# Optimization experiments

Hardware: AMD Instinct MI355X
Metric: run time of the kernel (lower is better)

Reference implementation:

```python
import jax, jax.numpy as jnp
import numpy as np
from jax import lax

L, D, V, T = 12, 1024, 50277, 1024
F4 = 4 * D


def setup_inputs() -> dict:
    key = jax.random.key(0)
    ks = jax.random.split(key, 20)
    s = 0.02  # weight scale keeps k (exp argument) well-conditioned
    n = lambda k, shape, scale=s: jax.random.normal(k, shape, dtype=jnp.float32) * scale
    u = lambda k, shape: jax.random.uniform(k, shape, dtype=jnp.float32)
    return {
        "tokens": jax.random.randint(ks[0], (T,), 0, V, dtype=jnp.int32),
        "emb": n(ks[1], (V, D), 1.0),
        "ln0_w": jnp.ones((D,), jnp.float32), "ln0_b": jnp.zeros((D,), jnp.float32),
        "ln1_w": jnp.ones((L, D), jnp.float32), "ln1_b": jnp.zeros((L, D), jnp.float32),
        "ln2_w": jnp.ones((L, D), jnp.float32), "ln2_b": jnp.zeros((L, D), jnp.float32),
        "tmk": u(ks[2], (L, D)), "tmv": u(ks[3], (L, D)), "tmr": u(ks[4], (L, D)),
        "tmk_ffn": u(ks[5], (L, D)), "tmr_ffn": u(ks[6], (L, D)),
        "time_first": n(ks[7], (L, D), 0.5),
        "time_decay": -jnp.exp(n(ks[8], (L, D), 0.5)),  # __init__: -exp(raw)
        "att_kw": n(ks[9], (L, D, D)), "att_vw": n(ks[10], (L, D, D)),
        "att_rw": n(ks[11], (L, D, D)), "att_ow": n(ks[12], (L, D, D)),
        "ffn_kw": n(ks[13], (L, D, F4)), "ffn_vw": n(ks[14], (L, F4, D)),
        "ffn_rw": n(ks[15], (L, D, D)),
        "lnout_w": jnp.ones((D,), jnp.float32), "lnout_b": jnp.zeros((D,), jnp.float32),
        "head": n(ks[16], (V, D)),
    }


def _ln(x, w, b):
    mu = jnp.mean(x, -1, keepdims=True)
    var = jnp.var(x, -1, keepdims=True)
    return (x - mu) / jnp.sqrt(var + 1e-5) * w + b


def _shift(x):  # token shift: prepend zero state row (state init is zeros)
    return jnp.concatenate([jnp.zeros_like(x[:1]), x[:-1]], axis=0)


def _wkv(k, v, tf, td):  # k,v: [T,D]; aa/bb/pp scan with running-max exp trick
    init = (jnp.zeros_like(k[0]), jnp.zeros_like(k[0]), jnp.full_like(k[0], -1e30))
    def step(c, kv):
        aa, bb, pp = c
        kt, vt = kv
        ww = tf + kt
        p = jnp.maximum(pp, ww)
        e1 = jnp.exp(pp - p); e2 = jnp.exp(ww - p)
        out = (e1 * aa + e2 * vt) / (e1 * bb + e2)
        ww2 = pp + td
        p2 = jnp.maximum(ww2, kt)
        e1 = jnp.exp(ww2 - p2); e2 = jnp.exp(kt - p2)
        return (e1 * aa + e2 * vt, e1 * bb + e2, p2), out
    _, out = lax.scan(step, init, (k, v))
    return out


def reference(tokens, emb, ln0_w, ln0_b, ln1_w, ln1_b, ln2_w, ln2_b, tmk, tmv, tmr,
              tmk_ffn, tmr_ffn, time_first, time_decay, att_kw, att_vw, att_rw, att_ow,
              ffn_kw, ffn_vw, ffn_rw, lnout_w, lnout_b, head):
    x = _ln(emb[tokens], ln0_w, ln0_b)  # [T,D]; ln0 applied to emb rows as in __init__
    for i in range(L):
        # time-mix (attention) block
        xn = _ln(x, ln1_w[i], ln1_b[i])
        xx = _shift(xn)
        xk = xn * tmk[i] + xx * (1 - tmk[i])
        xv = xn * tmv[i] + xx * (1 - tmv[i])
        xr = xn * tmr[i] + xx * (1 - tmr[i])
        r = jax.nn.sigmoid(xr @ att_rw[i])
        k = xk @ att_kw[i]
        v = xv @ att_vw[i]
        wkv = _wkv(k, v, time_first[i], time_decay[i])
        x = x + (r * wkv) @ att_ow[i]
        # channel-mix (ffn) block
        xn = _ln(x, ln2_w[i], ln2_b[i])
        xx = _shift(xn)
        xk = xn * tmk_ffn[i] + xx * (1 - tmk_ffn[i])
        xr = xn * tmr_ffn[i] + xx * (1 - tmr_ffn[i])
        rf = jax.nn.sigmoid(xr @ ffn_rw[i])
        kf = jnp.square(jax.nn.relu(xk @ ffn_kw[i]))
        x = x + rf * (kf @ ffn_vw[i])
    xo = _ln(x[-1], lnout_w, lnout_b)
    return head @ xo  # logits [V]
```

## Files before the change

kernel.cpp:

```cpp
#include <hip/hip_runtime.h>

#define Tn 1024
#define Dn 1024
#define Ln 12
#define F4n 4096
#define Vn 50277
#define TDn (Tn*Dn)
#define MEG 1048576
#define SEG 16
#define NSEG 64

typedef __attribute__((ext_vector_type(4))) float f4;
typedef __attribute__((ext_vector_type(16))) float f32x16;
typedef __attribute__((ext_vector_type(8))) short short8;
typedef unsigned short u16;
typedef unsigned int u32;
typedef __attribute__((ext_vector_type(4))) u16 us4;

#define ASG __attribute__((address_space(1)))
#define ASL __attribute__((address_space(3)))

__device__ __forceinline__ u16 f2b(float x){
  u32 u = __float_as_uint(x);
  return (u16)((u + 0x7fffu + ((u >> 16) & 1u)) >> 16);
}

__device__ __forceinline__ f4 blockReduce4(f4 v){
  __shared__ f4 s[4];
  int lane = threadIdx.x & 63, w = threadIdx.x >> 6;
#pragma unroll
  for(int o = 32; o; o >>= 1){
    v.x += __shfl_xor(v.x, o);
    v.y += __shfl_xor(v.y, o);
    v.z += __shfl_xor(v.z, o);
    v.w += __shfl_xor(v.w, o);
  }
  if(lane == 0) s[w] = v;
  __syncthreads();
  return s[0] + s[1] + s[2] + s[3];
}

struct ConvArgs {
  const float* s0; const float* s1; const float* s2; const float* s3;
  const float* skw;
  const float* svw;
  const float* srw;
  u16* dst;
};
__global__ __launch_bounds__(256) void conv_k(ConvArgs a){
  __shared__ u16 t[64][65];
  int b = blockIdx.x, tid = threadIdx.x;
  const float* src; u16* dst; int K, N, tk, tn;
  if(b < 1024){
    int m = b >> 8, bt = b & 255;
    src = (m==0)?a.s0:((m==1)?a.s1:((m==2)?a.s2:a.s3));
    dst = a.dst + (size_t)m*MEG; K=1024; N=1024; tk=bt>>4; tn=bt&15;
  } else if(b < 2048){
    int bt = b-1024; src=a.skw; dst=a.dst+(size_t)4*MEG; K=1024; N=4096; tk=bt>>6; tn=bt&63;
  } else if(b < 3072){
    int bt = b-2048; src=a.svw; dst=a.dst+(size_t)8*MEG; K=4096; N=1024; tk=bt>>4; tn=bt&15;
  } else {
    int bt = b-3072; src=a.srw; dst=a.dst+(size_t)12*MEG; K=1024; N=1024; tk=bt>>4; tn=bt&15;
  }
  int r0 = tid>>6, c = tid&63;
#pragma unroll
  for(int it=0; it<16; it++){
    int r = it*4 + r0;
    t[r][c] = f2b(src[(size_t)(tk*64+r)*N + tn*64 + c]);
  }
  __syncthreads();
  int n0 = tid>>4, k4 = (tid&15)*4;
#pragma unroll
  for(int it=0; it<4; it++){
    int n = it*16 + n0;
    us4 o; o[0]=t[k4][n]; o[1]=t[k4+1][n]; o[2]=t[k4+2][n]; o[3]=t[k4+3][n];
    *(us4*)&dst[(size_t)(tn*64+n)*K + tk*64 + k4] = o;
  }
}

__global__ __launch_bounds__(256) void embed_ln0_k(
    const int* __restrict__ tok, const float* __restrict__ emb,
    const float* __restrict__ w, const float* __restrict__ b,
    float* __restrict__ x){
  int t = blockIdx.x, tid = threadIdx.x;
  const f4* src = (const f4*)(emb + (size_t)tok[t] * Dn);
  f4 v = src[tid];
  f4 st;
  st.x = v.x+v.y+v.z+v.w;
  st.y = v.x*v.x+v.y*v.y+v.z*v.z+v.w*v.w;
  st.z = 0.f; st.w = 0.f;
  f4 red = blockReduce4(st);
  float mu = red.x * (1.0f/Dn);
  float rs = rsqrtf(red.y * (1.0f/Dn) - mu*mu + 1e-5f);
  f4 wv = ((const f4*)w)[tid], bv = ((const f4*)b)[tid];
  f4 o;
  o.x = (v.x-mu)*rs*wv.x + bv.x;
  o.y = (v.y-mu)*rs*wv.y + bv.y;
  o.z = (v.z-mu)*rs*wv.z + bv.z;
  o.w = (v.w-mu)*rs*wv.w + bv.w;
  ((f4*)(x + (size_t)t*Dn))[tid] = o;
}

__global__ __launch_bounds__(256) void ln_mix_att_k(
    const float* __restrict__ x,
    const float* __restrict__ lw, const float* __restrict__ lb,
    const float* __restrict__ tk, const float* __restrict__ tv, const float* __restrict__ tr,
    u16* __restrict__ xkvr){
  int t = blockIdx.x, tid = threadIdx.x;
  f4 cur = ((const f4*)(x + (size_t)t*Dn))[tid];
  f4 prv; prv.x=0.f; prv.y=0.f; prv.z=0.f; prv.w=0.f;
  if(t > 0) prv = ((const f4*)(x + (size_t)(t-1)*Dn))[tid];
  f4 st;
  st.x = cur.x+cur.y+cur.z+cur.w;
  st.y = cur.x*cur.x+cur.y*cur.y+cur.z*cur.z+cur.w*cur.w;
  st.z = prv.x+prv.y+prv.z+prv.w;
  st.w = prv.x*prv.x+prv.y*prv.y+prv.z*prv.z+prv.w*prv.w;
  f4 red = blockReduce4(st);
  float muc = red.x*(1.f/Dn), rsc = rsqrtf(red.y*(1.f/Dn)-muc*muc+1e-5f);
  float mup = red.z*(1.f/Dn), rsp = rsqrtf(red.w*(1.f/Dn)-mup*mup+1e-5f);
  f4 wv=((const f4*)lw)[tid], bv=((const f4*)lb)[tid];
  f4 kv=((const f4*)tk)[tid], vv=((const f4*)tv)[tid], rv=((const f4*)tr)[tid];
  us4 ok, ov, orr;
  float xn, xp;
#define MIX3(j, cj, pj, wj, bj, kj, vj, rj) \
  xn = (cj - muc)*rsc*wj + bj; \
  xp = (t>0) ? ((pj - mup)*rsp*wj + bj) : 0.f; \
  ok[j]  = f2b(xn*kj + xp*(1.f-kj)); \
  ov[j]  = f2b(xn*vj + xp*(1.f-vj)); \
  orr[j] = f2b(xn*rj + xp*(1.f-rj));
  MIX3(0, cur.x, prv.x, wv.x, bv.x, kv.x, vv.x, rv.x)
  MIX3(1, cur.y, prv.y, wv.y, bv.y, kv.y, vv.y, rv.y)
  MIX3(2, cur.z, prv.z, wv.z, bv.z, kv.z, vv.z, rv.z)
  MIX3(3, cur.w, prv.w, wv.w, bv.w, kv.w, vv.w, rv.w)
#undef MIX3
  size_t o0 = (size_t)t*Dn + tid*4;
  *(us4*)(xkvr + o0)         = ok;
  *(us4*)(xkvr + TDn + o0)   = ov;
  *(us4*)(xkvr + 2*TDn + o0) = orr;
}

__global__ __launch_bounds__(256) void ln_mix_ffn_k(
    const float* __restrict__ x,
    const float* __restrict__ lw, const float* __restrict__ lb,
    const float* __restrict__ tk, const float* __restrict__ tr,
    u16* __restrict__ xkr){
  int t = blockIdx.x, tid = threadIdx.x;
  f4 cur = ((const f4*)(x + (size_t)t*Dn))[tid];
  f4 prv; prv.x=0.f; prv.y=0.f; prv.z=0.f; prv.w=0.f;
  if(t > 0) prv = ((const f4*)(x + (size_t)(t-1)*Dn))[tid];
  f4 st;
  st.x = cur.x+cur.y+cur.z+cur.w;
  st.y = cur.x*cur.x+cur.y*cur.y+cur.z*cur.z+cur.w*cur.w;
  st.z = prv.x+prv.y+prv.z+prv.w;
  st.w = prv.x*prv.x+prv.y*prv.y+prv.z*prv.z+prv.w*prv.w;
  f4 red = blockReduce4(st);
  float muc = red.x*(1.f/Dn), rsc = rsqrtf(red.y*(1.f/Dn)-muc*muc+1e-5f);
  float mup = red.z*(1.f/Dn), rsp = rsqrtf(red.w*(1.f/Dn)-mup*mup+1e-5f);
  f4 wv=((const f4*)lw)[tid], bv=((const f4*)lb)[tid];
  f4 kv=((const f4*)tk)[tid], rv=((const f4*)tr)[tid];
  us4 ok, orr;
  float xn, xp;
#define MIX2(j, cj, pj, wj, bj, kj, rj) \
  xn = (cj - muc)*rsc*wj + bj; \
  xp = (t>0) ? ((pj - mup)*rsp*wj + bj) : 0.f; \
  ok[j]  = f2b(xn*kj + xp*(1.f-kj)); \
  orr[j] = f2b(xn*rj + xp*(1.f-rj));
  MIX2(0, cur.x, prv.x, wv.x, bv.x, kv.x, rv.x)
  MIX2(1, cur.y, prv.y, wv.y, bv.y, kv.y, rv.y)
  MIX2(2, cur.z, prv.z, wv.z, bv.z, kv.z, rv.z)
  MIX2(3, cur.w, prv.w, wv.w, bv.w, kv.w, rv.w)
#undef MIX2
  size_t o0 = (size_t)t*Dn + tid*4;
  *(us4*)(xkr + o0)       = ok;
  *(us4*)(xkr + TDn + o0) = orr;
}

__global__ __launch_bounds__(256) void wkv_seg_k(
    const float* __restrict__ kb, const float* __restrict__ vb,
    const float* __restrict__ tdp,
    float* __restrict__ sega, float* __restrict__ segb, float* __restrict__ segp){
  int ch = blockIdx.x*256 + threadIdx.x;
  int g = blockIdx.y;
  int t0 = g*SEG;
  float td = tdp[ch];
  float kk[SEG], vv[SEG];
#pragma unroll
  for(int j=0;j<SEG;j++){
    kk[j] = kb[(size_t)(t0+j)*Dn + ch];
    vv[j] = vb[(size_t)(t0+j)*Dn + ch];
  }
  float aa=0.f, bb=0.f, pp=-1e30f;
#pragma unroll
  for(int j=0;j<SEG;j++){
    float ww2 = pp + td;
    float p2 = fmaxf(ww2, kk[j]);
    float e1 = __expf(ww2-p2), e2 = __expf(kk[j]-p2);
    aa = e1*aa + e2*vv[j]; bb = e1*bb + e2; pp = p2;
  }
  size_t o = (size_t)g*Dn + ch;
  sega[o] = aa; segb[o] = bb; segp[o] = pp;
}

__global__ __launch_bounds__(256) void wkv_scan_k(
    const float* __restrict__ sega, const float* __restrict__ segb, const float* __restrict__ segp,
    const float* __restrict__ tdp,
    float* __restrict__ prea, float* __restrict__ preb, float* __restrict__ prep){
  int ch = blockIdx.x*256 + threadIdx.x;
  float Std = tdp[ch] * (float)SEG;
  float a=0.f, b=0.f, p=-1e30f;
  for(int g=0; g<NSEG; g++){
    size_t o = (size_t)g*Dn + ch;
    prea[o]=a; preb[o]=b; prep[o]=p;
    float ag=sega[o], bg=segb[o], qg=segp[o];
    float psh = p + Std;
    float pn = fmaxf(psh, qg);
    float eo = __expf(psh-pn), en = __expf(qg-pn);
    a = eo*a + en*ag; b = eo*b + en*bg; p = pn;
  }
}

__global__ __launch_bounds__(256) void wkv_out_k(
    const float* __restrict__ kb, const float* __restrict__ vb, const float* __restrict__ rb,
    const float* __restrict__ tfp, const float* __restrict__ tdp,
    const float* __restrict__ prea, const float* __restrict__ preb, const float* __restrict__ prep,
    u16* __restrict__ att_in){
  int ch = blockIdx.x*256 + threadIdx.x;
  int g = blockIdx.y;
  int t0 = g*SEG;
  float tf = tfp[ch], td = tdp[ch];
  size_t so = (size_t)g*Dn + ch;
  float aa = prea[so], bb = preb[so], pp = prep[so];
  float kk[SEG], vv[SEG], rr[SEG];
#pragma unroll
  for(int j=0;j<SEG;j++){
    kk[j]=kb[(size_t)(t0+j)*Dn+ch];
    vv[j]=vb[(size_t)(t0+j)*Dn+ch];
    rr[j]=rb[(size_t)(t0+j)*Dn+ch];
  }
#pragma unroll
  for(int j=0;j<SEG;j++){
    float kt=kk[j], vt=vv[j];
    float ww = tf + kt;
    float p = fmaxf(pp, ww);
    float e1 = __expf(pp-p), e2 = __expf(ww-p);
    float out = __fdividef(e1*aa+e2*vt, e1*bb+e2);
    float sig = __fdividef(1.f, 1.f+__expf(-rr[j]));
    att_in[(size_t)(t0+j)*Dn+ch] = f2b(sig*out);
    float ww2 = pp+td;
    float p2 = fmaxf(ww2,kt);
    e1 = __expf(ww2-p2); e2 = __expf(kt-p2);
    aa = e1*aa+e2*vt; bb = e1*bb+e2; pp = p2;
  }
}

template<int EPI>
__global__ __launch_bounds__(128) void gemm_k(
    const u16* __restrict__ A, size_t ldA, size_t strideA,
    const u16* __restrict__ Bt, size_t ldB, size_t strideB,
    int K, int N,
    float* __restrict__ Cf, size_t strideC, u16* __restrict__ Cb,
    const float* __restrict__ aux){
  __shared__ __align__(16) u16 lds[2][2][64*128];
  const int tid = threadIdx.x;
  const int l = tid & 63, w = tid >> 6;
  const int z = blockIdx.z;
  const u16* Az = A  + (size_t)z*strideA;
  const u16* Bz = Bt + (size_t)z*strideB;
  const int row0 = blockIdx.y*64, col0 = blockIdx.x*64;

  const u16* pA[8]; const u16* pB[8]; int ldsoff[8];
#pragma unroll
  for(int q=0;q<8;q++){
    int r = (q*2+w)*4 + (l>>4);
    int kk = (((l&15)*16) ^ ((r&15)<<4)) >> 1;
    pA[q] = Az + (size_t)(row0+r)*ldA + kk;
    pB[q] = Bz + (size_t)(col0+r)*ldB + kk;
    ldsoff[q] = (q*2+w)*512;
  }
  int foff[2][4];
#pragma unroll
  for(int i=0;i<2;i++){
    int row = i*32 + (l&31);
#pragma unroll
    for(int s=0;s<4;s++){
      int c = w*128 + s*32 + ((l>>5)*16);
      foff[i][s] = row*128 + ((c ^ ((row&15)<<4)) >> 1);
    }
  }

  f32x16 acc[2][2];
#pragma unroll
  for(int i=0;i<2;i++)
#pragma unroll
    for(int j=0;j<2;j++)
#pragma unroll
      for(int e=0;e<16;e++) acc[i][j][e] = 0.f;

#define STAGE(BUF) do{ \
  _Pragma("unroll") \
  for(int q=0;q<8;q++){ \
    __builtin_amdgcn_global_load_lds((ASG const void*)(const void*)pA[q], (ASL void*)(void*)&lds[BUF][0][ldsoff[q]], 16, 0, 0); \
    __builtin_amdgcn_global_load_lds((ASG const void*)(const void*)pB[q], (ASL void*)(void*)&lds[BUF][1][ldsoff[q]], 16, 0, 0); \
    pA[q] += 128; pB[q] += 128; \
  } }while(0)

  const int nss = K >> 7;
  STAGE(0);
  __syncthreads();
  int buf = 0;
  for(int ss=0; ss<nss; ss++){
    if(ss+1 < nss){
      if(buf) STAGE(0); else STAGE(1);
    }
    const u16* La = &lds[buf][0][0];
    const u16* Lb = &lds[buf][1][0];
#pragma unroll
    for(int s=0;s<4;s++){
      short8 a0 = *(const short8*)(La + foff[0][s]);
      short8 a1 = *(const short8*)(La + foff[1][s]);
      short8 b0 = *(const short8*)(Lb + foff[0][s]);
      short8 b1 = *(const short8*)(Lb + foff[1][s]);
      acc[0][0] = __builtin_amdgcn_mfma_f32_32x32x16_bf16(a0, b0, acc[0][0], 0, 0, 0);
      acc[0][1] = __builtin_amdgcn_mfma_f32_32x32x16_bf16(a0, b1, acc[0][1], 0, 0, 0);
      acc[1][0] = __builtin_amdgcn_mfma_f32_32x32x16_bf16(a1, b0, acc[1][0], 0, 0, 0);
      acc[1][1] = __builtin_amdgcn_mfma_f32_32x32x16_bf16(a1, b1, acc[1][1], 0, 0, 0);
    }
    __syncthreads();
    buf ^= 1;
  }
#undef STAGE

  float* red = (float*)&lds[0][0][0];
  if(w == 1){
#pragma unroll
    for(int i=0;i<2;i++)
#pragma unroll
      for(int j=0;j<2;j++)
#pragma unroll
        for(int reg=0;reg<16;reg++){
          int rr_ = (reg&3) + 8*(reg>>2) + 4*(l>>5);
          red[(size_t)(i*32 + rr_)*64 + j*32 + (l&31)] = acc[i][j][reg];
        }
  }
  __syncthreads();
  if(w == 0){
#pragma unroll
    for(int i=0;i<2;i++)
#pragma unroll
      for(int j=0;j<2;j++)
#pragma unroll
        for(int reg=0;reg<16;reg++){
          int rr_ = (reg&3) + 8*(reg>>2) + 4*(l>>5);
          float v = acc[i][j][reg] + red[(size_t)(i*32 + rr_)*64 + j*32 + (l&31)];
          int grow = row0 + i*32 + rr_;
          int gcol = col0 + j*32 + (l&31);
          size_t idx = (size_t)grow*N + gcol;
          if constexpr(EPI==0){ Cf[(size_t)z*strideC + idx] = v; }
          else if constexpr(EPI==1){ float t_ = v>0.f ? v : 0.f; Cb[idx] = f2b(t_*t_); }
          else if constexpr(EPI==2){ Cf[idx] += v; }
          else { float s_ = __fdividef(1.f, 1.f+__expf(-aux[idx])); Cf[idx] += s_*v; }
        }
  }
}

__global__ __launch_bounds__(256) void lnout_k(
    const float* __restrict__ x, const float* __restrict__ w, const float* __restrict__ b,
    float* __restrict__ xo){
  int tid = threadIdx.x;
  f4 v = ((const f4*)(x + (size_t)(Tn-1)*Dn))[tid];
  f4 st;
  st.x = v.x+v.y+v.z+v.w;
  st.y = v.x*v.x+v.y*v.y+v.z*v.z+v.w*v.w;
  st.z = 0.f; st.w = 0.f;
  f4 red = blockReduce4(st);
  float mu = red.x*(1.f/Dn);
  float rs = rsqrtf(red.y*(1.f/Dn) - mu*mu + 1e-5f);
  f4 wv = ((const f4*)w)[tid], bv = ((const f4*)b)[tid];
  f4 o;
  o.x = (v.x-mu)*rs*wv.x + bv.x;
  o.y = (v.y-mu)*rs*wv.y + bv.y;
  o.z = (v.z-mu)*rs*wv.z + bv.z;
  o.w = (v.w-mu)*rs*wv.w + bv.w;
  ((f4*)xo)[tid] = o;
}

__global__ __launch_bounds__(256) void head_k(
    const float* __restrict__ head, const float* __restrict__ xo, float* __restrict__ out){
  __shared__ f4 sxo[256];
  int tid = threadIdx.x;
  sxo[tid] = ((const f4*)xo)[tid];
  __syncthreads();
  int w = tid >> 6, lane = tid & 63;
  int row = blockIdx.x*4 + w;
  if(row < Vn){
    const f4* hr = (const f4*)(head + (size_t)row*Dn);
    float s = 0.f;
#pragma unroll
    for(int i=0;i<4;i++){
      f4 h = hr[i*64 + lane];
      f4 xv = sxo[i*64 + lane];
      s += h.x*xv.x + h.y*xv.y + h.z*xv.z + h.w*xv.w;
    }
#pragma unroll
    for(int o=32;o;o>>=1) s += __shfl_xor(s, o);
    if(lane == 0) out[row] = s;
  }
}

static inline void launch_gemm(int epi, dim3 grid,
    const u16* A, size_t ldA, size_t sA,
    const u16* Bt, size_t ldB, size_t sB,
    int K, int N,
    float* Cf, size_t sC, u16* Cb, const float* aux, hipStream_t s){
  switch(epi){
    case 0: gemm_k<0><<<grid, 128, 0, s>>>(A, ldA, sA, Bt, ldB, sB, K, N, Cf, sC, Cb, aux); break;
    case 1: gemm_k<1><<<grid, 128, 0, s>>>(A, ldA, sA, Bt, ldB, sB, K, N, Cf, sC, Cb, aux); break;
    case 2: gemm_k<2><<<grid, 128, 0, s>>>(A, ldA, sA, Bt, ldB, sB, K, N, Cf, sC, Cb, aux); break;
    default: gemm_k<3><<<grid, 128, 0, s>>>(A, ldA, sA, Bt, ldB, sB, K, N, Cf, sC, Cb, aux); break;
  }
}

extern "C" void kernel_launch(void* const* d_in, const int* in_sizes, int n_in,
                              void* d_out, int out_size, void* d_ws, size_t ws_size,
                              hipStream_t stream) {
  (void)in_sizes; (void)n_in; (void)out_size; (void)ws_size;
  const int*   tokens   = (const int*)  d_in[0];
  const float* emb      = (const float*)d_in[1];
  const float* ln0_w    = (const float*)d_in[2];
  const float* ln0_b    = (const float*)d_in[3];
  const float* ln1_w    = (const float*)d_in[4];
  const float* ln1_b    = (const float*)d_in[5];
  const float* ln2_w    = (const float*)d_in[6];
  const float* ln2_b    = (const float*)d_in[7];
  const float* tmk      = (const float*)d_in[8];
  const float* tmv      = (const float*)d_in[9];
  const float* tmr      = (const float*)d_in[10];
  const float* tmk_ffn  = (const float*)d_in[11];
  const float* tmr_ffn  = (const float*)d_in[12];
  const float* tfirst   = (const float*)d_in[13];
  const float* tdecay   = (const float*)d_in[14];
  const float* att_kw   = (const float*)d_in[15];
  const float* att_vw   = (const float*)d_in[16];
  const float* att_rw   = (const float*)d_in[17];
  const float* att_ow   = (const float*)d_in[18];
  const float* ffn_kw   = (const float*)d_in[19];
  const float* ffn_vw   = (const float*)d_in[20];
  const float* ffn_rw   = (const float*)d_in[21];
  const float* lnoutw   = (const float*)d_in[22];
  const float* lnoutb   = (const float*)d_in[23];
  const float* headw    = (const float*)d_in[24];
  float* logits = (float*)d_out;

  char* wsb = (char*)d_ws;
  size_t off = 0;
  auto carve = [&](size_t bytes)->void*{
    void* p = wsb + off;
    off += (bytes + 255) & ~(size_t)255;
    return p;
  };
  float* x      = (float*)carve((size_t)TDn*4);
  u16*   xkvr   = (u16*)  carve((size_t)3*TDn*2);
  float* kvr    = (float*)carve((size_t)3*TDn*4);
  u16*   att_in = (u16*)  carve((size_t)TDn*2);
  u16*   xkr    = (u16*)  carve((size_t)2*TDn*2);
  u16*   kf     = (u16*)  carve((size_t)Tn*F4n*2);
  float* rf     = (float*)carve((size_t)TDn*4);
  float* xo     = (float*)carve((size_t)Dn*4);
  u16*   wbt    = (u16*)  carve((size_t)13*MEG*2);
  float* sega   = (float*)carve((size_t)NSEG*Dn*4);
  float* segb   = (float*)carve((size_t)NSEG*Dn*4);
  float* segp   = (float*)carve((size_t)NSEG*Dn*4);
  float* prea   = (float*)carve((size_t)NSEG*Dn*4);
  float* preb   = (float*)carve((size_t)NSEG*Dn*4);
  float* prep   = (float*)carve((size_t)NSEG*Dn*4);

  embed_ln0_k<<<Tn, 256, 0, stream>>>(tokens, emb, ln0_w, ln0_b, x);

  for(int i=0;i<Ln;i++){
    size_t dd = (size_t)i*Dn*Dn;
    ConvArgs ca;
    ca.s0 = att_kw+dd; ca.s1 = att_vw+dd; ca.s2 = att_rw+dd; ca.s3 = att_ow+dd;
    ca.skw = ffn_kw+(size_t)i*Dn*F4n; ca.svw = ffn_vw+(size_t)i*F4n*Dn; ca.srw = ffn_rw+dd;
    ca.dst = wbt;
    conv_k<<<3328, 256, 0, stream>>>(ca);

    ln_mix_att_k<<<Tn, 256, 0, stream>>>(x, ln1_w+i*Dn, ln1_b+i*Dn,
                                         tmk+i*Dn, tmv+i*Dn, tmr+i*Dn, xkvr);
    launch_gemm(0, dim3(16,16,3), xkvr, Dn, (size_t)TDn,
                wbt, Dn, (size_t)MEG, Dn, Dn,
                kvr, (size_t)TDn, nullptr, nullptr, stream);
    wkv_seg_k<<<dim3(4,NSEG), 256, 0, stream>>>(kvr, kvr+TDn, tdecay+i*Dn, sega, segb, segp);
    wkv_scan_k<<<4, 256, 0, stream>>>(sega, segb, segp, tdecay+i*Dn, prea, preb, prep);
    wkv_out_k<<<dim3(4,NSEG), 256, 0, stream>>>(kvr, kvr+TDn, kvr+2*TDn,
                                                tfirst+i*Dn, tdecay+i*Dn,
                                                prea, preb, prep, att_in);
    launch_gemm(2, dim3(16,16,1), att_in, Dn, 0,
                wbt+(size_t)3*MEG, Dn, 0, Dn, Dn,
                x, 0, nullptr, nullptr, stream);
    ln_mix_ffn_k<<<Tn, 256, 0, stream>>>(x, ln2_w+i*Dn, ln2_b+i*Dn,
                                         tmk_ffn+i*Dn, tmr_ffn+i*Dn, xkr);
    launch_gemm(1, dim3(64,16,1), xkr, Dn, 0,
                wbt+(size_t)4*MEG, Dn, 0, Dn, F4n,
                nullptr, 0, kf, nullptr, stream);
    launch_gemm(0, dim3(16,16,1), xkr+TDn, Dn, 0,
                wbt+(size_t)12*MEG, Dn, 0, Dn, Dn,
                rf, 0, nullptr, nullptr, stream);
    launch_gemm(3, dim3(16,16,1), kf, F4n, 0,
                wbt+(size_t)8*MEG, F4n, 0, F4n, Dn,
                x, 0, nullptr, rf, stream);
  }

  lnout_k<<<1, 256, 0, stream>>>(x, lnoutw, lnoutb, xo);
  head_k<<<(Vn+3)/4, 256, 0, stream>>>(headw, xo, logits);
}
```

Measured before the change: 1.943 ms.

## Halve GEMM K-step to 64 and remap blocks for XCD-aware L2 locality

Shrinks the per-stage K tile in the bf16 MFMA GEMM from 128 to 64, halving LDS use per block, which may allow more resident blocks per CU. It also remaps the linear block index so that consecutive groups of column tiles land on the same one of 8 chiplets (XCDs). The goal is better L2 reuse of shared A/B tiles. The cost is twice as many K iterations and barriers per tile, and the remap assumes gridDim.x is divisible by 8.

```diff
diff --git a/kernel.cpp b/kernel.cpp
--- a/kernel.cpp
+++ b/kernel.cpp
@@ -260,31 +260,41 @@
     int K, int N,
     float* __restrict__ Cf, size_t strideC, u16* __restrict__ Cb,
     const float* __restrict__ aux){
-  __shared__ __align__(16) u16 lds[2][2][64*128];
+  __shared__ __align__(16) u16 lds[2][2][64*64];
   const int tid = threadIdx.x;
   const int l = tid & 63, w = tid >> 6;
-  const int z = blockIdx.z;
-  const u16* Az = A  + (size_t)z*strideA;
-  const u16* Bz = Bt + (size_t)z*strideB;
-  const int row0 = blockIdx.y*64, col0 = blockIdx.x*64;
-
-  const u16* pA[8]; const u16* pB[8]; int ldsoff[8];
-#pragma unroll
-  for(int q=0;q<8;q++){
-    int r = (q*2+w)*4 + (l>>4);
-    int kk = (((l&15)*16) ^ ((r&15)<<4)) >> 1;
+
+  const int GX = gridDim.x, GY = gridDim.y;
+  int lin = blockIdx.x + GX*(blockIdx.y + GY*blockIdx.z);
+  int c  = lin & 7, s = lin >> 3;
+  int XT = GX >> 3;
+  int tpz = XT * GY;
+  int tz  = s / tpz, rem = s - tz*tpz;
+  int tx  = c*XT + rem / GY;
+  int ty  = rem - (rem / GY)*GY;
+
+  const u16* Az = A  + (size_t)tz*strideA;
+  const u16* Bz = Bt + (size_t)tz*strideB;
+  const int row0 = ty*64, col0 = tx*64;
+
+  const u16* pA[4]; const u16* pB[4]; int ldsoff[4];
+#pragma unroll
+  for(int q=0;q<4;q++){
+    int ch = q*2 + w;
+    int r  = ch*8 + (l>>3);
+    int kk = ((((l&7)<<4) ^ ((l>>3)<<4)) >> 1);
     pA[q] = Az + (size_t)(row0+r)*ldA + kk;
     pB[q] = Bz + (size_t)(col0+r)*ldB + kk;
-    ldsoff[q] = (q*2+w)*512;
-  }
-  int foff[2][4];
+    ldsoff[q] = ch*512;
+  }
+  int foff[2][2];
 #pragma unroll
   for(int i=0;i<2;i++){
     int row = i*32 + (l&31);
 #pragma unroll
-    for(int s=0;s<4;s++){
-      int c = w*128 + s*32 + ((l>>5)*16);
-      foff[i][s] = row*128 + ((c ^ ((row&15)<<4)) >> 1);
+    for(int s2=0;s2<2;s2++){
+      int cb = w*64 + s2*32 + ((l>>5)*16);
+      foff[i][s2] = row*64 + ((cb ^ ((row&7)<<4)) >> 1);
     }
   }
 
@@ -298,13 +308,13 @@
 
 #define STAGE(BUF) do{ \
   _Pragma("unroll") \
-  for(int q=0;q<8;q++){ \
+  for(int q=0;q<4;q++){ \
     __builtin_amdgcn_global_load_lds((ASG const void*)(const void*)pA[q], (ASL void*)(void*)&lds[BUF][0][ldsoff[q]], 16, 0, 0); \
     __builtin_amdgcn_global_load_lds((ASG const void*)(const void*)pB[q], (ASL void*)(void*)&lds[BUF][1][ldsoff[q]], 16, 0, 0); \
-    pA[q] += 128; pB[q] += 128; \
+    pA[q] += 64; pB[q] += 64; \
   } }while(0)
 
-  const int nss = K >> 7;
+  const int nss = K >> 6;
   STAGE(0);
   __syncthreads();
   int buf = 0;
@@ -315,11 +325,11 @@
     const u16* La = &lds[buf][0][0];
     const u16* Lb = &lds[buf][1][0];
 #pragma unroll
-    for(int s=0;s<4;s++){
-      short8 a0 = *(const short8*)(La + foff[0][s]);
-      short8 a1 = *(const short8*)(La + foff[1][s]);
-      short8 b0 = *(const short8*)(Lb + foff[0][s]);
-      short8 b1 = *(const short8*)(Lb + foff[1][s]);
+    for(int s2=0;s2<2;s2++){
+      short8 a0 = *(const short8*)(La + foff[0][s2]);
+      short8 a1 = *(const short8*)(La + foff[1][s2]);
+      short8 b0 = *(const short8*)(Lb + foff[0][s2]);
+      short8 b1 = *(const short8*)(Lb + foff[1][s2]);
       acc[0][0] = __builtin_amdgcn_mfma_f32_32x32x16_bf16(a0, b0, acc[0][0], 0, 0, 0);
       acc[0][1] = __builtin_amdgcn_mfma_f32_32x32x16_bf16(a0, b1, acc[0][1], 0, 0, 0);
       acc[1][0] = __builtin_amdgcn_mfma_f32_32x32x16_bf16(a1, b0, acc[1][0], 0, 0, 0);
@@ -355,7 +365,7 @@
           int grow = row0 + i*32 + rr_;
           int gcol = col0 + j*32 + (l&31);
           size_t idx = (size_t)grow*N + gcol;
-          if constexpr(EPI==0){ Cf[(size_t)z*strideC + idx] = v; }
+          if constexpr(EPI==0){ Cf[(size_t)tz*strideC + idx] = v; }
           else if constexpr(EPI==1){ float t_ = v>0.f ? v : 0.f; Cb[idx] = f2b(t_*t_); }
           else if constexpr(EPI==2){ Cf[idx] += v; }
           else { float s_ = __fdividef(1.f, 1.f+__expf(-aux[idx])); Cf[idx] += s_*v; }
```

After: 2.018 ms. 3.8% more time.

## Batch weight conversion, fuse WKV scan into output, merge FFN key/receptance GEMMs

Applied to the files above, without the earlier changes.

Converts all twelve layers' weights to transposed bf16 in one launch before the layer loop, instead of one conversion launch per layer. The separate serial WKV segment-scan kernel is removed: each output block now recomputes its own prefix over earlier segments. The FFN key and receptance GEMMs run as a single launch with branch-selected epilogues. This cuts launch count and serialization, and raises occupancy for the small receptance GEMM. In exchange it needs a much larger bf16 weight workspace and adds redundant prefix-scan work that grows with segment index.

```diff
diff --git a/kernel.cpp b/kernel.cpp
--- a/kernel.cpp
+++ b/kernel.cpp
@@ -9,6 +9,7 @@
 #define MEG 1048576
 #define SEG 16
 #define NSEG 64
+#define WL (13*MEG)
 
 typedef __attribute__((ext_vector_type(4))) float f4;
 typedef __attribute__((ext_vector_type(16))) float f32x16;
@@ -41,26 +42,27 @@
 }
 
 struct ConvArgs {
-  const float* s0; const float* s1; const float* s2; const float* s3;
-  const float* skw;
-  const float* svw;
-  const float* srw;
+  const float* akw; const float* avw; const float* arw; const float* aow;
+  const float* fkw; const float* fvw; const float* frw;
   u16* dst;
 };
 __global__ __launch_bounds__(256) void conv_k(ConvArgs a){
   __shared__ u16 t[64][65];
-  int b = blockIdx.x, tid = threadIdx.x;
+  int b = blockIdx.x, L = blockIdx.y, tid = threadIdx.x;
   const float* src; u16* dst; int K, N, tk, tn;
+  size_t lyr_dd = (size_t)L*MEG;
+  size_t lyr_f4 = (size_t)L*4*MEG;
+  u16* dl = a.dst + (size_t)L*WL;
   if(b < 1024){
     int m = b >> 8, bt = b & 255;
-    src = (m==0)?a.s0:((m==1)?a.s1:((m==2)?a.s2:a.s3));
-    dst = a.dst + (size_t)m*MEG; K=1024; N=1024; tk=bt>>4; tn=bt&15;
+    src = ((m==0)?a.akw:((m==1)?a.avw:((m==2)?a.arw:a.aow))) + lyr_dd;
+    dst = dl + (size_t)m*MEG; K=1024; N=1024; tk=bt>>4; tn=bt&15;
   } else if(b < 2048){
-    int bt = b-1024; src=a.skw; dst=a.dst+(size_t)4*MEG; K=1024; N=4096; tk=bt>>6; tn=bt&63;
+    int bt = b-1024; src=a.fkw+lyr_f4; dst=dl+(size_t)4*MEG; K=1024; N=4096; tk=bt>>6; tn=bt&63;
   } else if(b < 3072){
-    int bt = b-2048; src=a.svw; dst=a.dst+(size_t)8*MEG; K=4096; N=1024; tk=bt>>4; tn=bt&15;
+    int bt = b-2048; src=a.fvw+lyr_f4; dst=dl+(size_t)8*MEG; K=4096; N=1024; tk=bt>>4; tn=bt&15;
   } else {
-    int bt = b-3072; src=a.srw; dst=a.dst+(size_t)12*MEG; K=1024; N=1024; tk=bt>>4; tn=bt&15;
+    int bt = b-3072; src=a.frw+lyr_dd; dst=dl+(size_t)12*MEG; K=1024; N=1024; tk=bt>>4; tn=bt&15;
   }
   int r0 = tid>>6, c = tid&63;
 #pragma unroll
@@ -201,35 +203,25 @@
   sega[o] = aa; segb[o] = bb; segp[o] = pp;
 }
 
-__global__ __launch_bounds__(256) void wkv_scan_k(
-    const float* __restrict__ sega, const float* __restrict__ segb, const float* __restrict__ segp,
-    const float* __restrict__ tdp,
-    float* __restrict__ prea, float* __restrict__ preb, float* __restrict__ prep){
-  int ch = blockIdx.x*256 + threadIdx.x;
-  float Std = tdp[ch] * (float)SEG;
-  float a=0.f, b=0.f, p=-1e30f;
-  for(int g=0; g<NSEG; g++){
-    size_t o = (size_t)g*Dn + ch;
-    prea[o]=a; preb[o]=b; prep[o]=p;
-    float ag=sega[o], bg=segb[o], qg=segp[o];
-    float psh = p + Std;
-    float pn = fmaxf(psh, qg);
-    float eo = __expf(psh-pn), en = __expf(qg-pn);
-    a = eo*a + en*ag; b = eo*b + en*bg; p = pn;
-  }
-}
-
-__global__ __launch_bounds__(256) void wkv_out_k(
+__global__ __launch_bounds__(256) void wkv_outscan_k(
     const float* __restrict__ kb, const float* __restrict__ vb, const float* __restrict__ rb,
     const float* __restrict__ tfp, const float* __restrict__ tdp,
-    const float* __restrict__ prea, const float* __restrict__ preb, const float* __restrict__ prep,
+    const float* __restrict__ sega, const float* __restrict__ segb, const float* __restrict__ segp,
     u16* __restrict__ att_in){
   int ch = blockIdx.x*256 + threadIdx.x;
   int g = blockIdx.y;
   int t0 = g*SEG;
   float tf = tfp[ch], td = tdp[ch];
-  size_t so = (size_t)g*Dn + ch;
-  float aa = prea[so], bb = preb[so], pp = prep[so];
+  float Std = td * (float)SEG;
+  float aa=0.f, bb=0.f, pp=-1e30f;
+  for(int j=0;j<g;j++){
+    size_t o = (size_t)j*Dn + ch;
+    float ag=sega[o], bg=segb[o], qg=segp[o];
+    float psh = pp + Std;
+    float pn = fmaxf(psh, qg);
+    float eo = __expf(psh-pn), en = __expf(qg-pn);
+    aa = eo*aa + en*ag; bb = eo*bb + en*bg; pp = pn;
+  }
   float kk[SEG], vv[SEG], rr[SEG];
 #pragma unroll
   for(int j=0;j<SEG;j++){
@@ -258,7 +250,7 @@
     const u16* __restrict__ A, size_t ldA, size_t strideA,
     const u16* __restrict__ Bt, size_t ldB, size_t strideB,
     int K, int N,
-    float* __restrict__ Cf, size_t strideC, u16* __restrict__ Cb,
+    float* __restrict__ Cf, size_t strideC,
     const float* __restrict__ aux){
   __shared__ __align__(16) u16 lds[2][2][64*128];
   const int tid = threadIdx.x;
@@ -356,9 +348,114 @@
           int gcol = col0 + j*32 + (l&31);
           size_t idx = (size_t)grow*N + gcol;
           if constexpr(EPI==0){ Cf[(size_t)z*strideC + idx] = v; }
-          else if constexpr(EPI==1){ float t_ = v>0.f ? v : 0.f; Cb[idx] = f2b(t_*t_); }
           else if constexpr(EPI==2){ Cf[idx] += v; }
           else { float s_ = __fdividef(1.f, 1.f+__expf(-aux[idx])); Cf[idx] += s_*v; }
+        }
+  }
+}
+
+__global__ __launch_bounds__(128) void gemm_fkr_k(
+    const u16* __restrict__ xkr, const u16* __restrict__ wl,
+    u16* __restrict__ kf, float* __restrict__ rf){
+  __shared__ __align__(16) u16 lds[2][2][64*128];
+  const int tid = threadIdx.x;
+  const int l = tid & 63, w = tid >> 6;
+  const bool isfk = blockIdx.x < 64;
+  const u16* Az = isfk ? xkr : xkr + TDn;
+  const u16* Bz = isfk ? wl + (size_t)4*MEG : wl + (size_t)12*MEG;
+  const int N = isfk ? F4n : Dn;
+  const int col0 = (isfk ? blockIdx.x : blockIdx.x-64)*64;
+  const int row0 = blockIdx.y*64;
+
+  const u16* pA[8]; const u16* pB[8]; int ldsoff[8];
+#pragma unroll
+  for(int q=0;q<8;q++){
+    int r = (q*2+w)*4 + (l>>4);
+    int kk = (((l&15)*16) ^ ((r&15)<<4)) >> 1;
+    pA[q] = Az + (size_t)(row0+r)*Dn + kk;
+    pB[q] = Bz + (size_t)(col0+r)*Dn + kk;
+    ldsoff[q] = (q*2+w)*512;
+  }
+  int foff[2][4];
+#pragma unroll
+  for(int i=0;i<2;i++){
+    int row = i*32 + (l&31);
+#pragma unroll
+    for(int s=0;s<4;s++){
+      int c = w*128 + s*32 + ((l>>5)*16);
+      foff[i][s] = row*128 + ((c ^ ((row&15)<<4)) >> 1);
+    }
+  }
+
+  f32x16 acc[2][2];
+#pragma unroll
+  for(int i=0;i<2;i++)
+#pragma unroll
+    for(int j=0;j<2;j++)
+#pragma unroll
+      for(int e=0;e<16;e++) acc[i][j][e] = 0.f;
+
+#define STAGE(BUF) do{ \
+  _Pragma("unroll") \
+  for(int q=0;q<8;q++){ \
+    __builtin_amdgcn_global_load_lds((ASG const void*)(const void*)pA[q], (ASL void*)(void*)&lds[BUF][0][ldsoff[q]], 16, 0, 0); \
+    __builtin_amdgcn_global_load_lds((ASG const void*)(const void*)pB[q], (ASL void*)(void*)&lds[BUF][1][ldsoff[q]], 16, 0, 0); \
+    pA[q] += 128; pB[q] += 128; \
+  } }while(0)
+
+  STAGE(0);
+  __syncthreads();
+  int buf = 0;
+#pragma unroll 1
+  for(int ss=0; ss<8; ss++){
+    if(ss+1 < 8){
+      if(buf) STAGE(0); else STAGE(1);
+    }
+    const u16* La = &lds[buf][0][0];
+    const u16* Lb = &lds[buf][1][0];
+#pragma unroll
+    for(int s=0;s<4;s++){
+      short8 a0 = *(const short8*)(La + foff[0][s]);
+      short8 a1 = *(const short8*)(La + foff[1][s]);
+      short8 b0 = *(const short8*)(Lb + foff[0][s]);
+      short8 b1 = *(const short8*)(Lb + foff[1][s]);
+      acc[0][0] = __builtin_amdgcn_mfma_f32_32x32x16_bf16(a0, b0, acc[0][0], 0, 0, 0);
+      acc[0][1] = __builtin_amdgcn_mfma_f32_32x32x16_bf16(a0, b1, acc[0][1], 0, 0, 0);
+      acc[1][0] = __builtin_amdgcn_mfma_f32_32x32x16_bf16(a1, b0, acc[1][0], 0, 0, 0);
+      acc[1][1] = __builtin_amdgcn_mfma_f32_32x32x16_bf16(a1, b1, acc[1][1], 0, 0, 0);
+    }
+    __syncthreads();
+    buf ^= 1;
+  }
+#undef STAGE
+
+  float* red = (float*)&lds[0][0][0];
+  if(w == 1){
+#pragma unroll
+    for(int i=0;i<2;i++)
+#pragma unroll
+      for(int j=0;j<2;j++)
+#pragma unroll
+        for(int reg=0;reg<16;reg++){
+          int rr_ = (reg&3) + 8*(reg>>2) + 4*(l>>5);
+          red[(size_t)(i*32 + rr_)*64 + j*32 + (l&31)] = acc[i][j][reg];
+        }
+  }
+  __syncthreads();
+  if(w == 0){
+#pragma unroll
+    for(int i=0;i<2;i++)
+#pragma unroll
+      for(int j=0;j<2;j++)
+#pragma unroll
+        for(int reg=0;reg<16;reg++){
+          int rr_ = (reg&3) + 8*(reg>>2) + 4*(l>>5);
+          float v = acc[i][j][reg] + red[(size_t)(i*32 + rr_)*64 + j*32 + (l&31)];
+          int grow = row0 + i*32 + rr_;
+          int gcol = col0 + j*32 + (l&31);
+          size_t idx = (size_t)grow*N + gcol;
+          if(isfk){ float t_ = v>0.f ? v : 0.f; kf[idx] = f2b(t_*t_); }
+          else rf[idx] = v;
         }
   }
 }
@@ -411,12 +508,11 @@
     const u16* A, size_t ldA, size_t sA,
     const u16* Bt, size_t ldB, size_t sB,
     int K, int N,
-    float* Cf, size_t sC, u16* Cb, const float* aux, hipStream_t s){
+    float* Cf, size_t sC, const float* aux, hipStream_t s){
   switch(epi){
-    case 0: gemm_k<0><<<grid, 128, 0, s>>>(A, ldA, sA, Bt, ldB, sB, K, N, Cf, sC, Cb, aux); break;
-    case 1: gemm_k<1><<<grid, 128, 0, s>>>(A, ldA, sA, Bt, ldB, sB, K, N, Cf, sC, Cb, aux); break;
-    case 2: gemm_k<2><<<grid, 128, 0, s>>>(A, ldA, sA, Bt, ldB, sB, K, N, Cf, sC, Cb, aux); break;
-    default: gemm_k<3><<<grid, 128, 0, s>>>(A, ldA, sA, Bt, ldB, sB, K, N, Cf, sC, Cb, aux); break;
+    case 0: gemm_k<0><<<grid, 128, 0, s>>>(A, ldA, sA, Bt, ldB, sB, K, N, Cf, sC, aux); break;
+    case 2: gemm_k<2><<<grid, 128, 0, s>>>(A, ldA, sA, Bt, ldB, sB, K, N, Cf, sC, aux); break;
+    default: gemm_k<3><<<grid, 128, 0, s>>>(A, ldA, sA, Bt, ldB, sB, K, N, Cf, sC, aux); break;
   }
 }
 
@@ -466,48 +562,38 @@
   u16*   kf     = (u16*)  carve((size_t)Tn*F4n*2);
   float* rf     = (float*)carve((size_t)TDn*4);
   float* xo     = (float*)carve((size_t)Dn*4);
-  u16*   wbt    = (u16*)  carve((size_t)13*MEG*2);
   float* sega   = (float*)carve((size_t)NSEG*Dn*4);
   float* segb   = (float*)carve((size_t)NSEG*Dn*4);
   float* segp   = (float*)carve((size_t)NSEG*Dn*4);
-  float* prea   = (float*)carve((size_t)NSEG*Dn*4);
-  float* preb   = (float*)carve((size_t)NSEG*Dn*4);
-  float* prep   = (float*)carve((size_t)NSEG*Dn*4);
+  u16*   wbt    = (u16*)  carve((size_t)Ln*WL*2);
+
+  ConvArgs ca;
+  ca.akw=att_kw; ca.avw=att_vw; ca.arw=att_rw; ca.aow=att_ow;
+  ca.fkw=ffn_kw; ca.fvw=ffn_vw; ca.frw=ffn_rw; ca.dst=wbt;
+  conv_k<<<dim3(3328, Ln), 256, 0, stream>>>(ca);
 
   embed_ln0_k<<<Tn, 256, 0, stream>>>(tokens, emb, ln0_w, ln0_b, x);
 
   for(int i=0;i<Ln;i++){
-    size_t dd = (size_t)i*Dn*Dn;
-    ConvArgs ca;
-    ca.s0 = att_kw+dd; ca.s1 = att_vw+dd; ca.s2 = att_rw+dd; ca.s3 = att_ow+dd;
-    ca.skw = ffn_kw+(size_t)i*Dn*F4n; ca.svw = ffn_vw+(size_t)i*F4n*Dn; ca.srw = ffn_rw+dd;
-    ca.dst = wbt;
-    conv_k<<<3328, 256, 0, stream>>>(ca);
-
+    u16* wl = wbt + (size_t)i*WL;
     ln_mix_att_k<<<Tn, 256, 0, stream>>>(x, ln1_w+i*Dn, ln1_b+i*Dn,
                                          tmk+i*Dn, tmv+i*Dn, tmr+i*Dn, xkvr);
     launch_gemm(0, dim3(16,16,3), xkvr, Dn, (size_t)TDn,
-                wbt, Dn, (size_t)MEG, Dn, Dn,
-                kvr, (size_t)TDn, nullptr, nullptr, stream);
+                wl, Dn, (size_t)MEG, Dn, Dn,
+                kvr, (size_t)TDn, nullptr, stream);
     wkv_seg_k<<<dim3(4,NSEG), 256, 0, stream>>>(kvr, kvr+TDn, tdecay+i*Dn, sega, segb, segp);
-    wkv_scan_k<<<4, 256, 0, stream>>>(sega, segb, segp, tdecay+i*Dn, prea, preb, prep);
-    wkv_out_k<<<dim3(4,NSEG), 256, 0, stream>>>(kvr, kvr+TDn, kvr+2*TDn,
-                                                tfirst+i*Dn, tdecay+i*Dn,
-                                                prea, preb, prep, att_in);
+    wkv_outscan_k<<<dim3(4,NSEG), 256, 0, stream>>>(kvr, kvr+TDn, kvr+2*TDn,
+                                                    tfirst+i*Dn, tdecay+i*Dn,
+                                                    sega, segb, segp, att_in);
     launch_gemm(2, dim3(16,16,1), att_in, Dn, 0,
-                wbt+(size_t)3*MEG, Dn, 0, Dn, Dn,
-                x, 0, nullptr, nullptr, stream);
+                wl+(size_t)3*MEG, Dn, 0, Dn, Dn,
+                x, 0, nullptr, stream);
     ln_mix_ffn_k<<<Tn, 256, 0, stream>>>(x, ln2_w+i*Dn, ln2_b+i*Dn,
                                          tmk_ffn+i*Dn, tmr_ffn+i*Dn, xkr);
-    launch_gemm(1, dim3(64,16,1), xkr, Dn, 0,
-                wbt+(size_t)4*MEG, Dn, 0, Dn, F4n,
-                nullptr, 0, kf, nullptr, stream);
-    launch_gemm(0, dim3(16,16,1), xkr+TDn, Dn, 0,
-                wbt+(size_t)12*MEG, Dn, 0, Dn, Dn,
-                rf, 0, nullptr, nullptr, stream);
+    gemm_fkr_k<<<dim3(80,16), 128, 0, stream>>>(xkr, wl, kf, rf);
     launch_gemm(3, dim3(16,16,1), kf, F4n, 0,
-                wbt+(size_t)8*MEG, F4n, 0, F4n, Dn,
-                x, 0, nullptr, rf, stream);
+                wl+(size_t)8*MEG, F4n, 0, F4n, Dn,
+                x, 0, rf, stream);
   }
 
   lnout_k<<<1, 256, 0, stream>>>(x, lnoutw, lnoutb, xo);
```

New measurement: 2.287 ms. +17.7%, slower.
